# Optimization experiments

Measured on AMD Instinct MI355X. Metric: run time of the kernel, lower is better.

## Reference

```python
import jax, jax.numpy as jnp
import numpy as np

N_NODES = 50000
N_EDGES = 800000
IN_C = 128
OUT_C = 128
HEADS = 1
BN_EPS = 1e-5


def setup_inputs() -> dict:
    key = jax.random.key(0)
    k1, k2, k3, k4, k5 = jax.random.split(key, 5)
    x = jax.random.normal(k1, (N_NODES, IN_C), dtype=jnp.float32)
    embedding = jax.random.normal(k2, (N_NODES, OUT_C), dtype=jnp.float32)
    # edges with no self loops (module strips then re-adds self loops)
    dst = jax.random.randint(k3, (N_EDGES,), 0, N_NODES)
    off = jax.random.randint(k4, (N_EDGES,), 1, N_NODES)
    src = (dst + off) % N_NODES
    edge_index = jnp.stack([src, dst]).astype(jnp.int64)
    # parameters
    W = jax.random.normal(k5, (HEADS * OUT_C, IN_C), dtype=jnp.float32) * (1.0 / np.sqrt(IN_C))
    bias = jnp.zeros((HEADS * OUT_C,), dtype=jnp.float32)
    gamma = jnp.ones((HEADS * OUT_C,), dtype=jnp.float32)
    beta = jnp.zeros((HEADS * OUT_C,), dtype=jnp.float32)
    return {"x": x, "edge_index": edge_index, "embedding": embedding,
            "W": W, "bias": bias, "gamma": gamma, "beta": beta}


def reference(x, edge_index, embedding, W, bias, gamma, beta):
    N = x.shape[0]
    xl = x @ W.T  # [N, H*C]
    # add self loops (input edges contain none)
    loop = jnp.arange(N, dtype=edge_index.dtype)
    src = jnp.concatenate([edge_index[0], loop])  # j (source)
    dst = jnp.concatenate([edge_index[1], loop])  # i (target / aggregation index)
    # per-edge attention: cosine-sim style embedding dot product (scalar, shared over heads)
    alpha = jnp.sum(embedding[dst] * embedding[src], axis=-1)  # [Etot]
    # segment softmax over destination neighborhoods
    amax = jax.ops.segment_max(alpha, dst, num_segments=N)
    e = jnp.exp(alpha - amax[dst])
    denom = jax.ops.segment_sum(e, dst, num_segments=N)
    a = e / (denom[dst] + 1e-16)  # [Etot]
    # gather-scale-scatter aggregation
    msg = xl[src] * a[:, None]  # [Etot, H*C]
    out = jax.ops.segment_sum(msg, dst, num_segments=N) + bias  # [N, H*C]
    # BatchNorm1d (training mode: batch stats, biased variance) + ReLU
    mu = out.mean(axis=0)
    var = jnp.mean((out - mu) ** 2, axis=0)
    out = (out - mu) * jax.lax.rsqrt(var + BN_EPS) * gamma + beta
    return jnp.maximum(out, 0.0)
```

## Files before the change

### kernel.cpp

```cpp
#include <hip/hip_runtime.h>
#include <math.h>

#define C 128

typedef _Float16 f16x8 __attribute__((ext_vector_type(8)));
typedef _Float16 half2_t __attribute__((ext_vector_type(2)));
typedef __attribute__((ext_vector_type(4))) float f32x4;

static __device__ __forceinline__ unsigned int pkh2(float lo, float hi) {
    unsigned short l = __builtin_bit_cast(unsigned short, (_Float16)lo);
    unsigned short h = __builtin_bit_cast(unsigned short, (_Float16)hi);
    return ((unsigned int)h << 16) | l;
}
static __device__ __forceinline__ float h2f_lo(unsigned int u) {
    return (float)__builtin_bit_cast(_Float16, (unsigned short)(u & 0xFFFFu));
}
static __device__ __forceinline__ float h2f_hi(unsigned int u) {
    return (float)__builtin_bit_cast(_Float16, (unsigned short)(u >> 16));
}
static __device__ __forceinline__ float dot2acc(unsigned int a, unsigned int b, float c) {
#if __has_builtin(__builtin_amdgcn_fdot2)
    return __builtin_amdgcn_fdot2(__builtin_bit_cast(half2_t, a),
                                  __builtin_bit_cast(half2_t, b), c, false);
#else
    c = fmaf(h2f_lo(a), h2f_lo(b), c);
    return fmaf(h2f_hi(a), h2f_hi(b), c);
#endif
}

__global__ __launch_bounds__(256) void k_stageA(const float* __restrict__ x,
                                                const float* __restrict__ Wf0,
                                                unsigned short* __restrict__ xlh,
                                                const float* __restrict__ embf,
                                                unsigned int* __restrict__ embh,
                                                const int* __restrict__ eidx,
                                                int* __restrict__ binCounts,
                                                int N, int E,
                                                int nGemmBlocks, int nCastBlocks,
                                                int totalA8) {
    __shared__ int lh[256];
    const int b = blockIdx.x;

    if (b < nGemmBlocks) {
        __shared__ unsigned int wsh[C * C / 2];
        const int tid = threadIdx.x;
        for (int i = tid; i < C * C / 8; i += 256) {
            const float4 a = ((const float4*)Wf0)[i * 2];
            const float4 bb = ((const float4*)Wf0)[i * 2 + 1];
            uint4 o;
            o.x = pkh2(a.x, a.y); o.y = pkh2(a.z, a.w);
            o.z = pkh2(bb.x, bb.y); o.w = pkh2(bb.z, bb.w);
            ((uint4*)wsh)[i] = o;
        }
        __syncthreads();

        const int lane = threadIdx.x & 63;
        const int wave = threadIdx.x >> 6;
        const int row0 = b * 64 + wave * 16;
        const int r = lane & 15, kg = lane >> 4;

        int arow = row0 + r;
        if (arow >= N) arow = N - 1;
        const float* xrow = x + (size_t)arow * C;
        f16x8 A[4];
#pragma unroll
        for (int kb = 0; kb < 4; ++kb) {
            const float4 p0 = ((const float4*)(xrow + kb * 32 + kg * 8))[0];
            const float4 p1 = ((const float4*)(xrow + kb * 32 + kg * 8))[1];
            f16x8 a;
            a[0] = (_Float16)p0.x; a[1] = (_Float16)p0.y;
            a[2] = (_Float16)p0.z; a[3] = (_Float16)p0.w;
            a[4] = (_Float16)p1.x; a[5] = (_Float16)p1.y;
            a[6] = (_Float16)p1.z; a[7] = (_Float16)p1.w;
            A[kb] = a;
        }

#pragma unroll
        for (int nt = 0; nt < 8; ++nt) {
            const uint4* wrow = (const uint4*)wsh + (size_t)(nt * 16 + r) * 16;
            f32x4 acc = {0.0f, 0.0f, 0.0f, 0.0f};
#pragma unroll
            for (int kb = 0; kb < 4; ++kb) {
                f16x8 B = __builtin_bit_cast(f16x8, wrow[kb * 4 + kg]);
                acc = __builtin_amdgcn_mfma_f32_16x16x32_f16(A[kb], B, acc, 0, 0, 0);
            }
            const int orow = row0 + kg * 4;
            const int ocol = nt * 16 + r;
#pragma unroll
            for (int i = 0; i < 4; ++i)
                if (orow + i < N)
                    xlh[(size_t)(orow + i) * C + ocol] =
                        __builtin_bit_cast(unsigned short, (_Float16)acc[i]);
        }
    } else if (b < nGemmBlocks + nCastBlocks) {
        int i = (b - nGemmBlocks) * 256 + threadIdx.x;
        if (i >= totalA8) return;
        const float4 a = ((const float4*)embf)[i * 2];
        const float4 bb = ((const float4*)embf)[i * 2 + 1];
        uint4 o;
        o.x = pkh2(a.x, a.y); o.y = pkh2(a.z, a.w);
        o.z = pkh2(bb.x, bb.y); o.w = pkh2(bb.z, bb.w);
        ((uint4*)embh)[i] = o;
    } else {
        const int t = threadIdx.x;
        lh[t] = 0;
        __syncthreads();
        const int base = (b - nGemmBlocks - nCastBlocks) * 2048;
#pragma unroll
        for (int j = 0; j < 8; ++j) {
            const int e = base + j * 256 + t;
            if (e < E) atomicAdd(&lh[eidx[E + e] >> 8], 1);
        }
        __syncthreads();
        const int v = lh[t];
        if (v) atomicAdd(&binCounts[t], v);
    }
}

__global__ __launch_bounds__(256) void k_bin(const int* __restrict__ eidx,
                                             const int* __restrict__ binCounts,
                                             int* __restrict__ binAlloc,
                                             unsigned int* __restrict__ binned, int E) {
    __shared__ int lh[256];
    __shared__ int sc[256];
    __shared__ int lb[256];
    const int t = threadIdx.x;
    const int v = binCounts[t];
    lh[t] = 0;
    sc[t] = v;
    __syncthreads();
    const int base = blockIdx.x * 2048;
    int bj[8], rj[8];
    unsigned int recj[8];
#pragma unroll
    for (int j = 0; j < 8; ++j) {
        const int e = base + j * 256 + t;
        bj[j] = -1;
        if (e < E) {
            const int s = eidx[e];
            const int d = eidx[E + e];
            bj[j] = d >> 8;
            recj[j] = ((unsigned)(d & 255) << 24) | (unsigned)s;
            rj[j] = atomicAdd(&lh[bj[j]], 1);
        }
    }
    __syncthreads();
    for (int o = 1; o < 256; o <<= 1) {
        int u = (t >= o) ? sc[t - o] : 0;
        __syncthreads();
        sc[t] += u;
        __syncthreads();
    }
    const int excl = sc[t] - v;
    const int c = lh[t];
    if (c) lb[t] = excl + atomicAdd(&binAlloc[t], c);
    __syncthreads();
#pragma unroll
    for (int j = 0; j < 8; ++j) {
        if (bj[j] >= 0) binned[lb[bj[j]] + rj[j]] = recj[j];
    }
}

__global__ __launch_bounds__(256) void k_place(const unsigned int* __restrict__ binned,
                                               const int* __restrict__ binCounts,
                                               int* __restrict__ offs,
                                               int* __restrict__ src_s,
                                               int N, int E, int NB) {
    __shared__ int sc[256];
    __shared__ int cnt[256];
    __shared__ int ts[256];
    __shared__ int cur[256];
    __shared__ int r0s, r1s;
    const int b = blockIdx.x;
    const int t = threadIdx.x;
    const int node0 = b * 256;
    const int v0 = binCounts[t];
    sc[t] = v0;
    cnt[t] = 0;
    __syncthreads();
    for (int o = 1; o < 256; o <<= 1) {
        int u = (t >= o) ? sc[t - o] : 0;
        __syncthreads();
        sc[t] += u;
        __syncthreads();
    }
    if (t == b) { r0s = sc[t] - v0; r1s = sc[t]; }
    __syncthreads();
    const int r0 = r0s, r1 = r1s;
    for (int i = r0 + t; i < r1; i += 256)
        atomicAdd(&cnt[binned[i] >> 24], 1);
    __syncthreads();
    const int v = cnt[t];
    ts[t] = v;
    __syncthreads();
    for (int o = 1; o < 256; o <<= 1) {
        int u = (t >= o) ? ts[t - o] : 0;
        __syncthreads();
        ts[t] += u;
        __syncthreads();
    }
    const int excl = r0 + ts[t] - v;
    if (node0 + t < N) offs[node0 + t] = excl;
    cur[t] = excl;
    __syncthreads();
    for (int i = r0 + t; i < r1; i += 256) {
        const unsigned int rec = binned[i];
        const int pos = atomicAdd(&cur[rec >> 24], 1);
        src_s[pos] = (int)(rec & 0xFFFFFFu);
    }
    if (b == NB - 1 && t == 0) offs[N] = E;
}

__global__ __launch_bounds__(256) void k_agg(const unsigned int* __restrict__ xlh,
                                             const unsigned int* __restrict__ embh,
                                             const int* __restrict__ src_s,
                                             const int* __restrict__ offs,
                                             const float* __restrict__ bias,
                                             float* __restrict__ out,
                                             float* __restrict__ psum,
                                             float* __restrict__ psq, int N) {
    const int node = (int)((blockIdx.x * (size_t)blockDim.x + threadIdx.x) >> 6);
    const int lane = threadIdx.x & 63;
    const int wave = threadIdx.x >> 6;
    const bool active = node < N;
    float2 o2 = {0.0f, 0.0f};

    if (active) {
        const int g = lane >> 3;
        const int sl = lane & 7;
        const int s0 = offs[node], s1 = offs[node + 1];

        const uint4* erow = (const uint4*)(embh + (size_t)node * (C / 2));
        const uint4 e0 = erow[sl * 2], e1 = erow[sl * 2 + 1];

        float p = 0.0f;
        p = dot2acc(e0.x, e0.x, p); p = dot2acc(e0.y, e0.y, p);
        p = dot2acc(e0.z, e0.z, p); p = dot2acc(e0.w, e0.w, p);
        p = dot2acc(e1.x, e1.x, p); p = dot2acc(e1.y, e1.y, p);
        p = dot2acc(e1.z, e1.z, p); p = dot2acc(e1.w, e1.w, p);
        p += __shfl_xor(p, 4); p += __shfl_xor(p, 2); p += __shfl_xor(p, 1);

        float m = p;
        float wself = 1.0f;
        float dex = 0.0f;
        float dpart = 0.0f;
        const unsigned int xw = xlh[(size_t)node * (C / 2) + lane];
        float2 acc = {h2f_lo(xw), h2f_hi(xw)};

        for (int base = s0; base < s1; base += 64) {
            int mys = -1;
            if (base + lane < s1) mys = src_s[base + lane];
            const int iters = min(8, (s1 - base + 7) >> 3);

            int sgc = __shfl(mys, g);
            {
                const int sac = (sgc >= 0) ? sgc : node;
            }
            const uint4* vrc = (const uint4*)(embh +
                                (size_t)((sgc >= 0) ? sgc : node) * (C / 2));
            uint4 v0c = vrc[sl * 2], v1c = vrc[sl * 2 + 1];

            for (int k = 0; k < iters; ++k) {
                int sgn = -1;
                uint4 v0n, v1n;
                if (k + 1 < iters) {
                    sgn = __shfl(mys, (k + 1) * 8 + g);
                    const uint4* vrn = (const uint4*)(embh +
                                        (size_t)((sgn >= 0) ? sgn : node) * (C / 2));
                    v0n = vrn[sl * 2];
                    v1n = vrn[sl * 2 + 1];
                }

                float a = 0.0f;
                a = dot2acc(e0.x, v0c.x, a); a = dot2acc(e0.y, v0c.y, a);
                a = dot2acc(e0.z, v0c.z, a); a = dot2acc(e0.w, v0c.w, a);
                a = dot2acc(e1.x, v1c.x, a); a = dot2acc(e1.y, v1c.y, a);
                a = dot2acc(e1.z, v1c.z, a); a = dot2acc(e1.w, v1c.w, a);
                a += __shfl_xor(a, 4); a += __shfl_xor(a, 2); a += __shfl_xor(a, 1);

                const bool valid = sgc >= 0;
                const bool hot = valid && (a > m - 28.0f);
                if (__any(hot)) {
                    const unsigned long long bal = __ballot(hot);
#pragma unroll 1
                    for (int j = 0; j < 8; ++j) {
                        if (!((bal >> (j * 8)) & 1ULL)) continue;
                        const float aj = __shfl(a, j * 8);
                        const int sj = __shfl(mys, k * 8 + j);
                        if (aj > m) {
                            const float cs = __expf(m - aj);
                            dpart *= cs; dex *= cs; wself *= cs;
                            acc.x *= cs; acc.y *= cs;
                            m = aj;
                        }
                        const float w = __expf(aj - m);
                        dex += w;
                        if (w > 1e-12f) {
                            const unsigned int u = xlh[(size_t)sj * (C / 2) + lane];
                            acc.x = fmaf(w, h2f_lo(u), acc.x);
                            acc.y = fmaf(w, h2f_hi(u), acc.y);
                        }
                    }
                }
                dpart += (valid && !hot) ? __expf(a - m) : 0.0f;

                sgc = sgn;
                v0c = v0n;
                v1c = v1n;
            }
        }

        float dg = dpart;
        dg += __shfl_xor(dg, 8); dg += __shfl_xor(dg, 16); dg += __shfl_xor(dg, 32);
        const float dtot = wself + dex + dg;
        const float inv = 1.0f / (dtot + 1e-16f);
        const int c = lane * 2;
        o2.x = fmaf(acc.x, inv, bias[c]);
        o2.y = fmaf(acc.y, inv, bias[c + 1]);
        ((float2*)(out + (size_t)node * C))[lane] = o2;
    }

    __shared__ float2 lsum[256];
    __shared__ float2 lsq[256];
    lsum[threadIdx.x] = o2;
    float2 q2v;
    q2v.x = o2.x * o2.x;
    q2v.y = o2.y * o2.y;
    lsq[threadIdx.x] = q2v;
    __syncthreads();
    if (wave == 0) {
        float2 S = lsum[lane], Q = lsq[lane];
#pragma unroll
        for (int j = 1; j < 4; ++j) {
            const float2 a = lsum[j * 64 + lane];
            const float2 b = lsq[j * 64 + lane];
            S.x += a.x; S.y += a.y;
            Q.x += b.x; Q.y += b.y;
        }
        const int slot = ((int)blockIdx.x & 63) * C + lane * 2;
        atomicAdd(&psum[slot],     S.x);
        atomicAdd(&psum[slot + 1], S.y);
        atomicAdd(&psq[slot],      Q.x);
        atomicAdd(&psq[slot + 1],  Q.y);
    }
}

__global__ __launch_bounds__(256) void k_bnapply(float* __restrict__ out,
                                                 const float* __restrict__ psum,
                                                 const float* __restrict__ psq,
                                                 const float* __restrict__ gamma,
                                                 const float* __restrict__ beta,
                                                 int N) {
    __shared__ float smu[C];
    __shared__ float ssc[C];
    __shared__ float sbe[C];
    const int t = threadIdx.x;
    if (t < C) {
        float S = 0.0f, Q = 0.0f;
#pragma unroll 4
        for (int b = 0; b < 64; ++b) {
            S += psum[b * C + t];
            Q += psq[b * C + t];
        }
        const float invN = 1.0f / (float)N;
        const float mu = S * invN;
        const float var = fmaxf(fmaf(-mu, mu, Q * invN), 0.0f);
        smu[t] = mu;
        ssc[t] = gamma[t] / sqrtf(var + 1e-5f);
        sbe[t] = beta[t];
    }
    __syncthreads();
    const int total4 = N * (C / 4);
    const int stride = (int)gridDim.x * 256;
    for (int idx = (int)blockIdx.x * 256 + t; idx < total4; idx += stride) {
        const int c = (idx * 4) & 127;
        float4 v = ((const float4*)out)[idx];
        float r[4] = {v.x, v.y, v.z, v.w};
#pragma unroll
        for (int j = 0; j < 4; ++j)
            r[j] = fmaxf(fmaf(r[j] - smu[c + j], ssc[c + j], sbe[c + j]), 0.0f);
        float4 o = {r[0], r[1], r[2], r[3]};
        ((float4*)out)[idx] = o;
    }
}

extern "C" void kernel_launch(void* const* d_in, const int* in_sizes, int n_in,
                              void* d_out, int out_size, void* d_ws, size_t ws_size,
                              hipStream_t stream) {
    const float* x     = (const float*)d_in[0];
    const int*   eidx  = (const int*)d_in[1];
    const float* emb   = (const float*)d_in[2];
    const float* W     = (const float*)d_in[3];
    const float* bias  = (const float*)d_in[4];
    const float* gamma = (const float*)d_in[5];
    const float* beta  = (const float*)d_in[6];
    const int N = in_sizes[0] / C;
    const int E = in_sizes[1] / 2;
    float* out = (float*)d_out;

    char* ws = (char*)d_ws;
    size_t off = 0;
    auto alloc = [&](size_t bytes) -> void* {
        void* p = ws + off;
        off = (off + bytes + 255) & ~(size_t)255;
        return p;
    };
    unsigned short* xlh  = (unsigned short*)alloc((size_t)N * C * 2);
    unsigned int*   embh = (unsigned int*)  alloc((size_t)N * C * 2);
    int*   src_s    = (int*)  alloc((size_t)E * 4);
    unsigned int* binned = (unsigned int*)alloc((size_t)E * 4);
    int*   offs     = (int*)  alloc((size_t)(N + 1) * 4);
    char*  zbase    = (char*)alloc(0);
    int*   binCounts= (int*)  alloc(256 * 4);
    int*   binAlloc = (int*)  alloc(256 * 4);
    float* psum     = (float*)alloc(64 * C * 4);
    float* psq      = (float*)alloc(64 * C * 4);
    size_t zbytes   = (char*)ws + off - zbase;

    const int NB = (N + 255) / 256;
    const int nEdgeBlocks = (E + 2047) / 2048;
    const int embTot8 = N * (C / 8);
    const int nGemmBlocks = (N + 63) / 64;
    const int nCastBlocks = (embTot8 + 255) / 256;

    hipMemsetAsync(zbase, 0, zbytes, stream);

    k_stageA <<<nGemmBlocks + nCastBlocks + nEdgeBlocks, 256, 0, stream>>>(
                 x, W, xlh, emb, embh, eidx, binCounts,
                 N, E, nGemmBlocks, nCastBlocks, embTot8);
    k_bin    <<<nEdgeBlocks,     256, 0, stream>>>(eidx, binCounts, binAlloc, binned, E);
    k_place  <<<NB,              256, 0, stream>>>(binned, binCounts, offs, src_s, N, E, NB);
    k_agg    <<<(int)(((size_t)N * 64 + 255) / 256), 256, 0, stream>>>(
                 (const unsigned int*)xlh, embh, src_s, offs, bias, out,
                 psum, psq, N);
    k_bnapply<<<512,             256, 0, stream>>>(out, psum, psq, gamma, beta, N);
}
```

Measured before the change: 117.7 us.

## Screen edge attention with int8 embeddings and exact fp32 recompute for hot edges

Embeddings are quantized to int8 (scale 16) instead of fp16, and the quantizer records the maximum per-chunk L1 norm and a clamp flag. The per-edge screening dot product becomes a 4-way int8 dot. An error bound derived from the L1 maximum decides which edges could matter; those are recomputed exactly in fp32 from the original embedding before the softmax update. This halves the bytes of embedding gathered per edge in the screening pass. In exchange it adds atomics in the cast stage and extra fp32 gathers for hot edges, and the skipped edges contribute an approximate weight to the denominator.

```diff
diff --git a/kernel.cpp b/kernel.cpp
--- a/kernel.cpp
+++ b/kernel.cpp
@@ -18,13 +18,15 @@
 static __device__ __forceinline__ float h2f_hi(unsigned int u) {
     return (float)__builtin_bit_cast(_Float16, (unsigned short)(u >> 16));
 }
-static __device__ __forceinline__ float dot2acc(unsigned int a, unsigned int b, float c) {
-#if __has_builtin(__builtin_amdgcn_fdot2)
-    return __builtin_amdgcn_fdot2(__builtin_bit_cast(half2_t, a),
-                                  __builtin_bit_cast(half2_t, b), c, false);
+static __device__ __forceinline__ int dot4i8(unsigned int a, unsigned int b, int c) {
+#if __has_builtin(__builtin_amdgcn_sdot4)
+    return __builtin_amdgcn_sdot4(a, b, c, false);
 #else
-    c = fmaf(h2f_lo(a), h2f_lo(b), c);
-    return fmaf(h2f_hi(a), h2f_hi(b), c);
+    c += (int)(signed char)(a & 0xff)         * (int)(signed char)(b & 0xff);
+    c += (int)(signed char)((a >> 8) & 0xff)  * (int)(signed char)((b >> 8) & 0xff);
+    c += (int)(signed char)((a >> 16) & 0xff) * (int)(signed char)((b >> 16) & 0xff);
+    c += (int)(signed char)((a >> 24) & 0xff) * (int)(signed char)((b >> 24) & 0xff);
+    return c;
 #endif
 }
 
@@ -32,7 +34,9 @@
                                                 const float* __restrict__ Wf0,
                                                 unsigned short* __restrict__ xlh,
                                                 const float* __restrict__ embf,
-                                                unsigned int* __restrict__ embh,
+                                                unsigned int* __restrict__ embq,
+                                                int* __restrict__ maxL1,
+                                                int* __restrict__ clampFlag,
                                                 const int* __restrict__ eidx,
                                                 int* __restrict__ binCounts,
                                                 int N, int E,
@@ -93,14 +97,33 @@
                         __builtin_bit_cast(unsigned short, (_Float16)acc[i]);
         }
     } else if (b < nGemmBlocks + nCastBlocks) {
-        int i = (b - nGemmBlocks) * 256 + threadIdx.x;
-        if (i >= totalA8) return;
-        const float4 a = ((const float4*)embf)[i * 2];
-        const float4 bb = ((const float4*)embf)[i * 2 + 1];
-        uint4 o;
-        o.x = pkh2(a.x, a.y); o.y = pkh2(a.z, a.w);
-        o.z = pkh2(bb.x, bb.y); o.w = pkh2(bb.z, bb.w);
-        ((uint4*)embh)[i] = o;
+        const int i = (b - nGemmBlocks) * 256 + threadIdx.x;
+        if (i < totalA8) {
+            const float4 a = ((const float4*)embf)[i * 2];
+            const float4 bb = ((const float4*)embf)[i * 2 + 1];
+            float v[8] = {a.x, a.y, a.z, a.w, bb.x, bb.y, bb.z, bb.w};
+            int q[8];
+            bool clamped = false;
+            float l1 = 0.0f;
+#pragma unroll
+            for (int j = 0; j < 8; ++j) {
+                l1 += fabsf(v[j]);
+                int qi = __float2int_rn(v[j] * 16.0f);
+                if (qi > 127 || qi < -127) { clamped = true; }
+                q[j] = max(-127, min(127, qi));
+            }
+            uint2 o;
+            o.x = (unsigned)(q[0] & 255) | ((unsigned)(q[1] & 255) << 8) |
+                  ((unsigned)(q[2] & 255) << 16) | ((unsigned)(q[3] & 255) << 24);
+            o.y = (unsigned)(q[4] & 255) | ((unsigned)(q[5] & 255) << 8) |
+                  ((unsigned)(q[6] & 255) << 16) | ((unsigned)(q[7] & 255) << 24);
+            ((uint2*)embq)[i] = o;
+#pragma unroll
+            for (int o2 = 8; o2 >= 1; o2 >>= 1) l1 += __shfl_xor(l1, o2);
+            if ((threadIdx.x & 15) == 0)
+                atomicMax(maxL1, __float_as_int(l1));
+            if (clamped) atomicOr(clampFlag, 1);
+        }
     } else {
         const int t = threadIdx.x;
         lh[t] = 0;
@@ -212,10 +235,13 @@
 }
 
 __global__ __launch_bounds__(256) void k_agg(const unsigned int* __restrict__ xlh,
-                                             const unsigned int* __restrict__ embh,
+                                             const float* __restrict__ emb,
+                                             const uint4* __restrict__ embq4,
                                              const int* __restrict__ src_s,
                                              const int* __restrict__ offs,
                                              const float* __restrict__ bias,
+                                             const int* __restrict__ maxL1,
+                                             const int* __restrict__ clampFlag,
                                              float* __restrict__ out,
                                              float* __restrict__ psum,
                                              float* __restrict__ psq, int N) {
@@ -230,70 +256,81 @@
         const int sl = lane & 7;
         const int s0 = offs[node], s1 = offs[node + 1];
 
-        const uint4* erow = (const uint4*)(embh + (size_t)node * (C / 2));
-        const uint4 e0 = erow[sl * 2], e1 = erow[sl * 2 + 1];
-
-        float p = 0.0f;
-        p = dot2acc(e0.x, e0.x, p); p = dot2acc(e0.y, e0.y, p);
-        p = dot2acc(e0.z, e0.z, p); p = dot2acc(e0.w, e0.w, p);
-        p = dot2acc(e1.x, e1.x, p); p = dot2acc(e1.y, e1.y, p);
-        p = dot2acc(e1.z, e1.z, p); p = dot2acc(e1.w, e1.w, p);
-        p += __shfl_xor(p, 4); p += __shfl_xor(p, 2); p += __shfl_xor(p, 1);
-
-        float m = p;
+        const float M = __int_as_float(*maxL1);
+        const float DELTA = M * 0.0625f + 0.25f;
+        const bool allhot = (*clampFlag) != 0;
+
+        float m;
+        {
+            const float4* er = (const float4*)(emb + (size_t)node * C) + sl * 4;
+            float p = 0.0f;
+#pragma unroll
+            for (int k = 0; k < 4; ++k) {
+                const float4 v = er[k];
+                p = fmaf(v.x, v.x, p); p = fmaf(v.y, v.y, p);
+                p = fmaf(v.z, v.z, p); p = fmaf(v.w, v.w, p);
+            }
+            p += __shfl_xor(p, 4); p += __shfl_xor(p, 2); p += __shfl_xor(p, 1);
+            m = p;
+        }
+
         float wself = 1.0f;
         float dex = 0.0f;
         float dpart = 0.0f;
         const unsigned int xw = xlh[(size_t)node * (C / 2) + lane];
         float2 acc = {h2f_lo(xw), h2f_hi(xw)};
 
+        const uint4 qd = embq4[(size_t)node * 8 + sl];
+
         for (int base = s0; base < s1; base += 64) {
             int mys = -1;
             if (base + lane < s1) mys = src_s[base + lane];
             const int iters = min(8, (s1 - base + 7) >> 3);
 
             int sgc = __shfl(mys, g);
-            {
-                const int sac = (sgc >= 0) ? sgc : node;
-            }
-            const uint4* vrc = (const uint4*)(embh +
-                                (size_t)((sgc >= 0) ? sgc : node) * (C / 2));
-            uint4 v0c = vrc[sl * 2], v1c = vrc[sl * 2 + 1];
+            uint4 qc = embq4[(size_t)((sgc >= 0) ? sgc : node) * 8 + sl];
 
             for (int k = 0; k < iters; ++k) {
                 int sgn = -1;
-                uint4 v0n, v1n;
+                uint4 qn;
                 if (k + 1 < iters) {
                     sgn = __shfl(mys, (k + 1) * 8 + g);
-                    const uint4* vrn = (const uint4*)(embh +
-                                        (size_t)((sgn >= 0) ? sgn : node) * (C / 2));
-                    v0n = vrn[sl * 2];
-                    v1n = vrn[sl * 2 + 1];
+                    qn = embq4[(size_t)((sgn >= 0) ? sgn : node) * 8 + sl];
                 }
 
-                float a = 0.0f;
-                a = dot2acc(e0.x, v0c.x, a); a = dot2acc(e0.y, v0c.y, a);
-                a = dot2acc(e0.z, v0c.z, a); a = dot2acc(e0.w, v0c.w, a);
-                a = dot2acc(e1.x, v1c.x, a); a = dot2acc(e1.y, v1c.y, a);
-                a = dot2acc(e1.z, v1c.z, a); a = dot2acc(e1.w, v1c.w, a);
-                a += __shfl_xor(a, 4); a += __shfl_xor(a, 2); a += __shfl_xor(a, 1);
+                int ai = dot4i8(qc.x, qd.x, 0);
+                ai = dot4i8(qc.y, qd.y, ai);
+                ai = dot4i8(qc.z, qd.z, ai);
+                ai = dot4i8(qc.w, qd.w, ai);
+                ai += __shfl_xor(ai, 4); ai += __shfl_xor(ai, 2); ai += __shfl_xor(ai, 1);
+                const float af = (float)ai * 0.00390625f;
 
                 const bool valid = sgc >= 0;
-                const bool hot = valid && (a > m - 28.0f);
+                const bool hot = valid && (allhot || (af + DELTA > m - 28.0f));
                 if (__any(hot)) {
                     const unsigned long long bal = __ballot(hot);
 #pragma unroll 1
                     for (int j = 0; j < 8; ++j) {
                         if (!((bal >> (j * 8)) & 1ULL)) continue;
-                        const float aj = __shfl(a, j * 8);
                         const int sj = __shfl(mys, k * 8 + j);
-                        if (aj > m) {
-                            const float cs = __expf(m - aj);
+                        const float4* dr = (const float4*)(emb + (size_t)node * C) + sl * 4;
+                        const float4* sr = (const float4*)(emb + (size_t)sj * C) + sl * 4;
+                        float ax = 0.0f;
+#pragma unroll
+                        for (int kk = 0; kk < 4; ++kk) {
+                            const float4 dv = dr[kk];
+                            const float4 sv = sr[kk];
+                            ax = fmaf(dv.x, sv.x, ax); ax = fmaf(dv.y, sv.y, ax);
+                            ax = fmaf(dv.z, sv.z, ax); ax = fmaf(dv.w, sv.w, ax);
+                        }
+                        ax += __shfl_xor(ax, 4); ax += __shfl_xor(ax, 2); ax += __shfl_xor(ax, 1);
+                        if (ax > m) {
+                            const float cs = __expf(m - ax);
                             dpart *= cs; dex *= cs; wself *= cs;
                             acc.x *= cs; acc.y *= cs;
-                            m = aj;
+                            m = ax;
                         }
-                        const float w = __expf(aj - m);
+                        const float w = __expf(ax - m);
                         dex += w;
                         if (w > 1e-12f) {
                             const unsigned int u = xlh[(size_t)sj * (C / 2) + lane];
@@ -302,11 +339,10 @@
                         }
                     }
                 }
-                dpart += (valid && !hot) ? __expf(a - m) : 0.0f;
+                dpart += (valid && !hot) ? __expf(af - m) : 0.0f;
 
                 sgc = sgn;
-                v0c = v0n;
-                v1c = v1n;
+                qc = qn;
             }
         }
 
@@ -406,7 +442,7 @@
         return p;
     };
     unsigned short* xlh  = (unsigned short*)alloc((size_t)N * C * 2);
-    unsigned int*   embh = (unsigned int*)  alloc((size_t)N * C * 2);
+    unsigned int*   embq = (unsigned int*)  alloc((size_t)N * C);
     int*   src_s    = (int*)  alloc((size_t)E * 4);
     unsigned int* binned = (unsigned int*)alloc((size_t)E * 4);
     int*   offs     = (int*)  alloc((size_t)(N + 1) * 4);
@@ -415,6 +451,8 @@
     int*   binAlloc = (int*)  alloc(256 * 4);
     float* psum     = (float*)alloc(64 * C * 4);
     float* psq      = (float*)alloc(64 * C * 4);
+    int*   maxL1    = (int*)  alloc(4);
+    int*   clampFlag= (int*)  alloc(4);
     size_t zbytes   = (char*)ws + off - zbase;
 
     const int NB = (N + 255) / 256;
@@ -426,12 +464,12 @@
     hipMemsetAsync(zbase, 0, zbytes, stream);
 
     k_stageA <<<nGemmBlocks + nCastBlocks + nEdgeBlocks, 256, 0, stream>>>(
-                 x, W, xlh, emb, embh, eidx, binCounts,
+                 x, W, xlh, emb, embq, maxL1, clampFlag, eidx, binCounts,
                  N, E, nGemmBlocks, nCastBlocks, embTot8);
     k_bin    <<<nEdgeBlocks,     256, 0, stream>>>(eidx, binCounts, binAlloc, binned, E);
     k_place  <<<NB,              256, 0, stream>>>(binned, binCounts, offs, src_s, N, E, NB);
     k_agg    <<<(int)(((size_t)N * 64 + 255) / 256), 256, 0, stream>>>(
-                 (const unsigned int*)xlh, embh, src_s, offs, bias, out,
-                 psum, psq, N);
+                 (const unsigned int*)xlh, emb, (const uint4*)embq,
+                 src_s, offs, bias, maxL1, clampFlag, out, psum, psq, N);
     k_bnapply<<<512,             256, 0, stream>>>(out, psum, psq, gamma, beta, N);
 }
```

After: 242.3 us. 2.06x slower.
